# Kernel tuning notes

Hardware: AMD Instinct MI355X
Metric: run time of the kernel (lower is better)

The kernel has to match this reference:

```python
import jax, jax.numpy as jnp
import numpy as np

K = 3
PAD = 1


def conv2d(x, w, b, pad):
    y = jax.lax.conv_general_dilated(
        x, w, window_strides=(1, 1), padding=[(pad, pad), (pad, pad)],
        dimension_numbers=("NCHW", "OIHW", "NCHW"))
    return y + b[None, :, None, None]


def dcn_v2(f, w_off, b_off, w, b):
    # Modulated deformable conv (DCNv2), stride=1, pad=1, dilation=1, dg=1.
    B, C, H, W = f.shape
    om = conv2d(f, w_off, b_off, PAD)                 # [B, 27, H, W]
    o1, o2, m = jnp.split(om, 3, axis=1)
    offset = jnp.concatenate([o1, o2], axis=1).reshape(B, K * K, 2, H, W)
    dy, dx = offset[:, :, 0], offset[:, :, 1]          # [B, 9, H, W]
    mask = jax.nn.sigmoid(m)                           # [B, 9, H, W]
    ky = (jnp.arange(K * K) // K).astype(f.dtype)      # kernel row per tap
    kx = (jnp.arange(K * K) % K).astype(f.dtype)       # kernel col per tap
    hh = jnp.arange(H, dtype=f.dtype)
    ww = jnp.arange(W, dtype=f.dtype)
    ys = hh[None, None, :, None] - PAD + ky[None, :, None, None] + dy  # [B,9,H,W]
    xs = ww[None, None, None, :] - PAD + kx[None, :, None, None] + dx
    y0 = jnp.floor(ys)
    x0 = jnp.floor(xs)
    wy1 = ys - y0
    wx1 = xs - x0
    wy0 = 1.0 - wy1
    wx0 = 1.0 - wx1
    f_flat = f.reshape(B, C, H * W)

    def gather(yi, xi):
        valid = (yi >= 0) & (yi <= H - 1) & (xi >= 0) & (xi <= W - 1)
        yc = jnp.clip(yi, 0, H - 1).astype(jnp.int32)
        xc = jnp.clip(xi, 0, W - 1).astype(jnp.int32)
        idx = (yc * W + xc).reshape(B, 1, -1)          # [B,1,9*H*W]
        g = jnp.take_along_axis(f_flat, idx, axis=2).reshape(B, C, K * K, H, W)
        return g * valid.astype(f.dtype).reshape(B, 1, K * K, H, W)

    v = (gather(y0, x0) * (wy0 * wx0)[:, None]
         + gather(y0, x0 + 1) * (wy0 * wx1)[:, None]
         + gather(y0 + 1, x0) * (wy1 * wx0)[:, None]
         + gather(y0 + 1, x0 + 1) * (wy1 * wx1)[:, None])   # [B,C,9,H,W]
    v = v * mask[:, None]
    out = jnp.einsum("bckhw,ock->bohw", v, w.reshape(w.shape[0], C, K * K))
    return out + b[None, :, None, None]


def setup_inputs() -> dict:
    key = jax.random.key(0)
    ks = jax.random.split(key, 10)
    B, C, H, W = 2, 256, 128, 128
    s = 0.05
    return {
        "x": jax.random.normal(ks[0], (B, C, H, W), jnp.float32),
        "votes": jax.random.normal(ks[1], (B, C, H, W), jnp.float32),
        "w1": jax.random.normal(ks[2], (C, C, 3, 3), jnp.float32) * s,
        "b1": jnp.zeros((C,), jnp.float32),
        "w_off": jax.random.normal(ks[3], (27, C, 3, 3), jnp.float32) * 0.01,
        "b_off": jnp.zeros((27,), jnp.float32),
        "w_dcn": jax.random.normal(ks[4], (C, C, 3, 3), jnp.float32) * s,
        "b_dcn": jnp.zeros((C,), jnp.float32),
        "w2": jax.random.normal(ks[5], (C, C, 3, 3), jnp.float32) * s,
        "b2": jnp.zeros((C,), jnp.float32),
        "w3": jax.random.normal(ks[6], (C, C, 3, 3), jnp.float32) * s,
        "b3": jnp.zeros((C,), jnp.float32),
        "w4": jax.random.normal(ks[7], (2, C, 1, 1), jnp.float32) * s,
        "b4": jnp.zeros((2,), jnp.float32),
    }


def reference(x, votes, w1, b1, w_off, b_off, w_dcn, b_dcn, w2, b2, w3, b3, w4, b4):
    v = jax.nn.relu(votes)
    t = jax.nn.relu(conv2d(v, w1, b1, PAD))            # conv3x3 + relu
    t = jax.nn.relu(dcn_v2(t, w_off, b_off, w_dcn, b_dcn))  # DCN + relu
    t = conv2d(t, w2, b2, PAD)                         # conv3x3 (no relu)
    g = t * x                                          # gated by x
    h = jax.nn.relu(conv2d(g, w3, b3, PAD))            # conv3x3 + relu
    out = conv2d(h, w4, b4, 0)                         # 1x1 -> outplanes
    return out
```

## Files before the change

### kernel.cpp

```cpp
#include <hip/hip_runtime.h>
#include <math.h>

typedef short short8 __attribute__((ext_vector_type(8)));
typedef float f32x4 __attribute__((ext_vector_type(4)));
typedef unsigned int uint4v __attribute__((ext_vector_type(4)));
typedef unsigned short ushort_t;

__device__ inline ushort_t f2bf(float f) {
    unsigned u = __builtin_bit_cast(unsigned, f);
    u = (u + 0x7fffu + ((u >> 16) & 1u)) >> 16;
    return (ushort_t)u;
}
__device__ inline float bf2f(ushort_t u) {
    return __builtin_bit_cast(float, (unsigned)u << 16);
}
__device__ inline void gload_lds16(const ushort_t* g, short* l) {
    __builtin_amdgcn_global_load_lds((const __attribute__((address_space(1))) unsigned int*)g,
                                     (__attribute__((address_space(3))) unsigned int*)l, 16, 0, 0);
}

__device__ inline void wpack_body(const float* __restrict__ w, ushort_t* __restrict__ wpk,
                                  int COUT, int NF, int bidLocal, int tid) {
    int T = bidLocal * 256 + tid;
    int lane = T & 63;
    int rest = T >> 6;
    int n = rest % NF;
    int kstep = rest / NF;
    int t = kstep >> 3, cc = kstep & 7;
    int oc = n * 16 + (lane & 15);
    int kk = (lane >> 4) * 8;
    short8 sv;
#pragma unroll
    for (int j = 0; j < 8; ++j) {
        int ci = cc * 32 + kk + j;
        float val = (oc < COUT) ? w[((size_t)oc * 256 + ci) * 9 + t] : 0.f;
        sv[j] = (short)f2bf(val);
    }
    *(short8*)&wpk[(size_t)T * 8] = sv;
}

__global__ __launch_bounds__(256)
void prep_all_kernel(const float* w1, ushort_t* wpk1,
                     const float* w_off, ushort_t* wpkO,
                     const float* w_dcn, ushort_t* wpkD,
                     const float* w2, ushort_t* wpk2,
                     const float* w3, ushort_t* wpk3,
                     ushort_t* zp,
                     const float* __restrict__ votes, const float* __restrict__ x,
                     ushort_t* __restrict__ aN, ushort_t* __restrict__ xN) {
    __shared__ short s[64 * 66];
    int bid = blockIdx.x, tid = threadIdx.x;
    if (bid < 288)       { wpack_body(w1,    wpk1, 256, 16, bid,        tid); return; }
    else if (bid < 324)  { wpack_body(w_off, wpkO, 27,  2,  bid - 288,  tid); return; }
    else if (bid < 612)  { wpack_body(w_dcn, wpkD, 256, 16, bid - 324,  tid); return; }
    else if (bid < 900)  { wpack_body(w2,    wpk2, 256, 16, bid - 612,  tid); return; }
    else if (bid < 1188) { wpack_body(w3,    wpk3, 256, 16, bid - 900,  tid); return; }
    else if (bid == 1188) { zp[tid] = 0; return; }
    int nb = bid - 1189;
    const int px0 = (nb & 255) * 64;
    const int ci0 = ((nb >> 8) & 3) * 64;
    const int z   = nb >> 10;
    const int b   = z & 1;
    const bool doRelu = (z < 2);
    const float* inb = (doRelu ? votes : x) + (size_t)b * 256 * 16384;
    ushort_t* ob = (doRelu ? aN : xN) + (size_t)b * 16384 * 256;
#pragma unroll
    for (int rep = 0; rep < 16; ++rep) {
        int cl = rep * 4 + (tid >> 6);
        int pl = tid & 63;
        float v = inb[(size_t)(ci0 + cl) * 16384 + px0 + pl];
        if (doRelu) v = fmaxf(v, 0.f);
        s[pl * 66 + cl] = (short)f2bf(v);
    }
    __syncthreads();
#pragma unroll
    for (int rep = 0; rep < 2; ++rep) {
        int c = rep * 256 + tid;
        int pl = c >> 3;
        int cl = (c & 7) * 8;
        *(short8*)&ob[(size_t)(px0 + pl) * 256 + ci0 + cl] = *(const short8*)&s[pl * 66 + cl];
    }
}

template<int TW, int OUTC, int EPI>
__global__ __launch_bounds__(512, 2)
void conv_mfma_kernel(const ushort_t* __restrict__ in, const ushort_t* __restrict__ wpk,
                      const float* __restrict__ bias, int coutReal,
                      const ushort_t* __restrict__ xin, ushort_t* __restrict__ outp,
                      const ushort_t* __restrict__ zp,
                      const float* __restrict__ w4g, const float* __restrict__ b4g,
                      float* __restrict__ out4)
{
    constexpr int NF = OUTC / 16;
    constexpr int NN = (NF < 4) ? NF : 4;
    constexpr int HWD = TW + 2;
    constexpr int HPX = 6 * HWD;
    constexpr int ROUNDS = (HPX * 4 + 511) / 512;
    constexpr int MW  = TW / 16;
    constexpr int MPW = TW / 8;
    constexpr int PITCH = OUTC + 4;
    union SM { short a[2][ROUNDS * 512 * 8]; float e[TW * PITCH]; };
    __shared__ __align__(16) SM sm;

    const int tid  = threadIdx.x;
    const int lane = tid & 63;
    const int wv   = tid >> 6;
    const int hi   = lane >> 4;
    const int lo   = lane & 15;
    const int pxg  = wv & 1;
    const int wn   = wv >> 1;
    const int wnu  = __builtin_amdgcn_readfirstlane(wn);
    const int x0 = blockIdx.x * TW;
    const int y0 = blockIdx.y * 4;
    const int b  = blockIdx.z;
    const ushort_t* inb = in + (size_t)b * 16384 * 256;

    const ushort_t* sptr[ROUNDS];
    int sstep[ROUNDS];
#pragma unroll
    for (int r = 0; r < ROUNDS; ++r) {
        int g = r * 512 + tid;
        int px = g >> 2, slot = g & 3;
        int hy = px / HWD, hx = px - hy * HWD;
        int gy = y0 - 1 + hy, gx = x0 - 1 + hx;
        bool ok = (px < HPX) && ((unsigned)gy < 128u) && ((unsigned)gx < 128u);
        int kk = (px ^ (px >> 2)) & 3;
        sptr[r] = ok ? (inb + (size_t)((gy << 7) + gx) * 256 + ((slot ^ kk) << 3))
                     : (zp + (slot << 3));
        sstep[r] = ok ? 32 : 0;
    }

    int pxh_base[MPW];
#pragma unroll
    for (int m = 0; m < MPW; ++m)
        pxh_base[m] = (2 * pxg + m / MW) * HWD + (m % MW) * 16 + lo;

    f32x4 acc[MPW][NN];
#pragma unroll
    for (int m = 0; m < MPW; ++m)
#pragma unroll
        for (int n = 0; n < NN; ++n) acc[m][n] = (f32x4){0.f, 0.f, 0.f, 0.f};

#pragma unroll
    for (int r = 0; r < ROUNDS; ++r)
        gload_lds16(sptr[r], &sm.a[0][(r * 512 + wv * 64) * 8]);
    __syncthreads();

    for (int cc = 0; cc < 8; ++cc) {
        const int buf = cc & 1;
        if (cc < 7) {
#pragma unroll
            for (int r = 0; r < ROUNDS; ++r)
                gload_lds16(sptr[r] + (size_t)(cc + 1) * sstep[r],
                            &sm.a[buf ^ 1][(r * 512 + wv * 64) * 8]);
        }
        if (NF >= 4 || wnu == 0) {
#pragma unroll
            for (int t = 0; t < 9; ++t) {
                const int ky = t / 3, kx = t % 3;
                short8 bf[NN];
#pragma unroll
                for (int n = 0; n < NN; ++n)
                    bf[n] = *(const short8*)&wpk[((size_t)((t * 8 + cc) * NF + wnu * NN + n) * 64 + lane) * 8];
                short8 af[MPW];
#pragma unroll
                for (int m = 0; m < MPW; ++m) {
                    int ph = pxh_base[m] + ky * HWD + kx;
                    int off = ph * 32 + ((hi ^ ((ph ^ (ph >> 2)) & 3)) << 3);
                    af[m] = *(const short8*)&sm.a[buf][off];
                }
#pragma unroll
                for (int m = 0; m < MPW; ++m)
#pragma unroll
                    for (int n = 0; n < NN; ++n)
                        acc[m][n] = __builtin_amdgcn_mfma_f32_16x16x32_bf16(af[m], bf[n], acc[m][n], 0, 0, 0);
            }
        }
        __syncthreads();
    }

    float br[NN];
#pragma unroll
    for (int n = 0; n < NN; ++n) {
        int oc = wn * (16 * NN) + n * 16 + lo;
        br[n] = (oc < coutReal) ? bias[oc] : 0.f;
    }
    const size_t obase = ((size_t)b * 16384 + (size_t)y0 * 128 + x0) * OUTC;
#pragma unroll
    for (int p = 0; p < 4; ++p) {
        if (pxg == (p >> 1) && (NF >= 4 || wnu == 0)) {
#pragma unroll
            for (int mm = 0; mm < MW; ++mm) {
                int m = (p & 1) * MW + mm;
#pragma unroll
                for (int n = 0; n < NN; ++n)
#pragma unroll
                    for (int r = 0; r < 4; ++r) {
                        int col = mm * 16 + hi * 4 + r;
                        float v = acc[m][n][r] + br[n];
                        if (EPI == 1 || EPI == 3) v = fmaxf(v, 0.f);
                        sm.e[col * PITCH + wn * (16 * NN) + n * 16 + lo] = v;
                    }
            }
        }
        __syncthreads();
        if constexpr (EPI == 3) {
            int col = tid >> 5;
            int ch  = tid & 31;
            f32x4 v0 = *(const f32x4*)&sm.e[col * PITCH + ch * 8];
            f32x4 v1 = *(const f32x4*)&sm.e[col * PITCH + ch * 8 + 4];
            float4 wa0 = *(const float4*)&w4g[ch * 8];
            float4 wa1 = *(const float4*)&w4g[ch * 8 + 4];
            float4 wb0 = *(const float4*)&w4g[256 + ch * 8];
            float4 wb1 = *(const float4*)&w4g[256 + ch * 8 + 4];
            float a0 = v0[0] * wa0.x + v0[1] * wa0.y + v0[2] * wa0.z + v0[3] * wa0.w
                     + v1[0] * wa1.x + v1[1] * wa1.y + v1[2] * wa1.z + v1[3] * wa1.w;
            float a1 = v0[0] * wb0.x + v0[1] * wb0.y + v0[2] * wb0.z + v0[3] * wb0.w
                     + v1[0] * wb1.x + v1[1] * wb1.y + v1[2] * wb1.z + v1[3] * wb1.w;
#pragma unroll
            for (int s = 16; s >= 1; s >>= 1) {
                a0 += __shfl_xor(a0, s);
                a1 += __shfl_xor(a1, s);
            }
            if (ch == 0) {
                size_t o = (size_t)b * 2 * 16384 + (size_t)(y0 + p) * 128 + x0 + col;
                out4[o]         = a0 + b4g[0];
                out4[o + 16384] = a1 + b4g[1];
            }
        } else {
            constexpr int CHUNKS = TW * OUTC / 8;
            for (int c = tid; c < CHUNKS; c += 512) {
                int col = c / (OUTC / 8);
                int ch = c % (OUTC / 8);
                f32x4 v0 = *(const f32x4*)&sm.e[col * PITCH + ch * 8];
                f32x4 v1 = *(const f32x4*)&sm.e[col * PITCH + ch * 8 + 4];
                size_t gidx = obase + ((size_t)p * 128 + col) * OUTC + ch * 8;
                if (EPI == 2) {
                    uint4v xu = *(const uint4v*)&xin[gidx];
#pragma unroll
                    for (int j = 0; j < 4; ++j) {
                        float xa = bf2f((ushort_t)(xu[j] & 0xffffu));
                        float xb = __builtin_bit_cast(float, xu[j] & 0xffff0000u);
                        if (j < 2) { v0[2 * j] *= xa; v0[2 * j + 1] *= xb; }
                        else       { v1[2 * (j - 2)] *= xa; v1[2 * (j - 2) + 1] *= xb; }
                    }
                }
                short8 s;
#pragma unroll
                for (int j = 0; j < 4; ++j) s[j] = (short)f2bf(v0[j]);
#pragma unroll
                for (int j = 0; j < 4; ++j) s[4 + j] = (short)f2bf(v1[j]);
                *(short8*)&outp[gidx] = s;
            }
        }
        __syncthreads();
    }
}

__device__ inline void corner8(uint4v u, float w, float* sv) {
#pragma unroll
    for (int j = 0; j < 4; ++j) {
        unsigned a = u[j];
        sv[2 * j]     = fmaf(w, __builtin_bit_cast(float, a << 16), sv[2 * j]);
        sv[2 * j + 1] = fmaf(w, __builtin_bit_cast(float, a & 0xffff0000u), sv[2 * j + 1]);
    }
}

__global__ __launch_bounds__(256, 2)
void dcn_mfma_kernel(const ushort_t* __restrict__ ft, const ushort_t* __restrict__ omt,
                     const ushort_t* __restrict__ wpk, const float* __restrict__ bias,
                     ushort_t* __restrict__ outp)
{
    union SM { short a[2][2][2048]; float e[16 * 264]; };
    __shared__ __align__(16) SM sm;

    const int tid  = threadIdx.x;
    const int lane = tid & 63;
    const int wv   = tid >> 6;
    const int hi   = lane >> 4;
    const int lo   = lane & 15;
    const int bid  = blockIdx.x;
    const int tile = (bid & 7) * 64 + (bid >> 3);
    const int b    = tile >> 8;
    const int rem  = tile & 255;
    const int y0   = (rem >> 3) * 4;
    const int x0   = (rem & 7) * 16;
    const ushort_t* fb = ft + (size_t)b * 16384 * 256;

    const int pxl = (wv << 4) | (lane >> 2);
    const int q   = lane & 3;

    float mw[9][4];
    unsigned mc[9];
    {
        const int py = y0 + (pxl >> 4), pxx = x0 + (pxl & 15);
        const ushort_t* omp = omt + ((size_t)b * 16384 + py * 128 + pxx) * 32;
        uint4v ow[4];
#pragma unroll
        for (int j = 0; j < 4; ++j) ow[j] = *(const uint4v*)(omp + j * 8);
        unsigned wbuf[14];
#pragma unroll
        for (int j = 0; j < 4; ++j)
#pragma unroll
            for (int e = 0; e < 4; ++e)
                if (j * 4 + e < 14) wbuf[j * 4 + e] = ow[j][e];
#pragma unroll
        for (int t = 0; t < 9; ++t) {
            float dy = bf2f((ushort_t)(wbuf[t] & 0xffffu));
            float dx = bf2f((ushort_t)(wbuf[t] >> 16));
            unsigned mw_ = wbuf[(18 + t) >> 1];
            float mr = ((18 + t) & 1) ? bf2f((ushort_t)(mw_ >> 16)) : bf2f((ushort_t)(mw_ & 0xffffu));
            float mk = 1.f / (1.f + expf(-mr));
            float ys = (float)(py - 1 + t / 3) + dy;
            float xs = (float)(pxx - 1 + t % 3) + dx;
            float y0f = floorf(ys), x0f = floorf(xs);
            float wy1 = ys - y0f, wx1 = xs - x0f;
            float wy0 = 1.f - wy1, wx0 = 1.f - wx1;
            int yi = (int)y0f, xi = (int)x0f;
            bool vy0 = (yi >= 0) && (yi < 128), vy1 = (yi + 1 >= 0) && (yi + 1 < 128);
            bool vx0 = (xi >= 0) && (xi < 128), vx1 = (xi + 1 >= 0) && (xi + 1 < 128);
            mw[t][0] = (vy0 && vx0) ? wy0 * wx0 * mk : 0.f;
            mw[t][1] = (vy0 && vx1) ? wy0 * wx1 * mk : 0.f;
            mw[t][2] = (vy1 && vx0) ? wy1 * wx0 * mk : 0.f;
            mw[t][3] = (vy1 && vx1) ? wy1 * wx1 * mk : 0.f;
            int y0c = min(max(yi, 0), 127), y1c = min(max(yi + 1, 0), 127);
            int x0c = min(max(xi, 0), 127), x1c = min(max(xi + 1, 0), 127);
            mc[t] = (unsigned)y0c | ((unsigned)y1c << 8) | ((unsigned)x0c << 16) | ((unsigned)x1c << 24);
        }
    }

    const int w_off = pxl * 32 + ((q ^ ((pxl ^ (pxl >> 2)) & 3)) << 3);
    int a_off[4];
#pragma unroll
    for (int m = 0; m < 4; ++m) {
        int p_ = m * 16 + lo;
        a_off[m] = p_ * 32 + ((hi ^ ((p_ ^ (p_ >> 2)) & 3)) << 3);
    }

    f32x4 acc[4][4];
#pragma unroll
    for (int m = 0; m < 4; ++m)
#pragma unroll
        for (int n = 0; n < 4; ++n) acc[m][n] = (f32x4){0.f, 0.f, 0.f, 0.f};

    uint4v n0a, n0b, n0c, n0d;
    uint4v n1a, n1b, n1c, n1d;

    {
        unsigned c = mc[0];
        int yy0 = c & 255, yy1 = (c >> 8) & 255, xx0 = (c >> 16) & 255, xx1 = c >> 24;
        size_t o00 = (size_t)((yy0 << 7) + xx0) * 256, o01 = (size_t)((yy0 << 7) + xx1) * 256;
        size_t o10 = (size_t)((yy1 << 7) + xx0) * 256, o11 = (size_t)((yy1 << 7) + xx1) * 256;
#pragma unroll
        for (int h = 0; h < 2; ++h) {
            const ushort_t* pc = fb + h * 32 + q * 8;
            uint4v g0 = *(const uint4v*)(pc + o00);
            uint4v g1 = *(const uint4v*)(pc + o01);
            uint4v g2 = *(const uint4v*)(pc + o10);
            uint4v g3 = *(const uint4v*)(pc + o11);
            float sv[8] = {0.f, 0.f, 0.f, 0.f, 0.f, 0.f, 0.f, 0.f};
            corner8(g0, mw[0][0], sv); corner8(g1, mw[0][1], sv);
            corner8(g2, mw[0][2], sv); corner8(g3, mw[0][3], sv);
            unsigned pk[4];
#pragma unroll
            for (int j = 0; j < 4; ++j)
                asm("v_cvt_pk_bf16_f32 %0, %1, %2" : "=v"(pk[j]) : "v"(sv[2 * j]), "v"(sv[2 * j + 1]));
            *(uint4v*)&sm.a[0][h][w_off] = (uint4v){pk[0], pk[1], pk[2], pk[3]};
        }
    }
    __syncthreads();

    for (int cch = 0; cch < 4; ++cch) {
#pragma unroll
        for (int t = 0; t < 9; ++t) {
            const int cur = (cch + t) & 1;
            const bool last = (cch == 3) && (t == 8);
            const int tn   = (t == 8) ? 0 : t + 1;
            const int cchn = (t == 8) ? cch + 1 : cch;
            if (!last) {
                unsigned c = mc[tn];
                int yy0 = c & 255, yy1 = (c >> 8) & 255, xx0 = (c >> 16) & 255, xx1 = c >> 24;
                size_t o00 = (size_t)((yy0 << 7) + xx0) * 256, o01 = (size_t)((yy0 << 7) + xx1) * 256;
                size_t o10 = (size_t)((yy1 << 7) + xx0) * 256, o11 = (size_t)((yy1 << 7) + xx1) * 256;
                const ushort_t* pc0 = fb + (2 * cchn) * 32 + q * 8;
                n0a = *(const uint4v*)(pc0 + o00);
                n0b = *(const uint4v*)(pc0 + o01);
                n0c = *(const uint4v*)(pc0 + o10);
                n0d = *(const uint4v*)(pc0 + o11);
                const ushort_t* pc1 = pc0 + 32;
                n1a = *(const uint4v*)(pc1 + o00);
                n1b = *(const uint4v*)(pc1 + o01);
                n1c = *(const uint4v*)(pc1 + o10);
                n1d = *(const uint4v*)(pc1 + o11);
            }
            short8 bfr0[4], bfr1[4];
            {
                const ushort_t* bs0 = wpk + ((size_t)((t * 8 + 2 * cch) * 16 + wv * 4) * 64 + lane) * 8;
#pragma unroll
                for (int n = 0; n < 4; ++n)
                    bfr0[n] = *(const short8*)(bs0 + (size_t)n * 512);
                const ushort_t* bs1 = bs0 + 16 * 512;
#pragma unroll
                for (int n = 0; n < 4; ++n)
                    bfr1[n] = *(const short8*)(bs1 + (size_t)n * 512);
            }
#pragma unroll
            for (int m = 0; m < 4; ++m) {
                short8 af0 = *(const short8*)&sm.a[cur][0][a_off[m]];
                short8 af1 = *(const short8*)&sm.a[cur][1][a_off[m]];
#pragma unroll
                for (int n = 0; n < 4; ++n)
                    acc[m][n] = __builtin_amdgcn_mfma_f32_16x16x32_bf16(af0, bfr0[n], acc[m][n], 0, 0, 0);
#pragma unroll
                for (int n = 0; n < 4; ++n)
                    acc[m][n] = __builtin_amdgcn_mfma_f32_16x16x32_bf16(af1, bfr1[n], acc[m][n], 0, 0, 0);
            }
            if (!last) {
                {
                    float sv[8] = {0.f, 0.f, 0.f, 0.f, 0.f, 0.f, 0.f, 0.f};
                    corner8(n0a, mw[tn][0], sv); corner8(n0b, mw[tn][1], sv);
                    corner8(n0c, mw[tn][2], sv); corner8(n0d, mw[tn][3], sv);
                    unsigned pk[4];
#pragma unroll
                    for (int j = 0; j < 4; ++j)
                        asm("v_cvt_pk_bf16_f32 %0, %1, %2" : "=v"(pk[j]) : "v"(sv[2 * j]), "v"(sv[2 * j + 1]));
                    *(uint4v*)&sm.a[cur ^ 1][0][w_off] = (uint4v){pk[0], pk[1], pk[2], pk[3]};
                }
                {
                    float sv[8] = {0.f, 0.f, 0.f, 0.f, 0.f, 0.f, 0.f, 0.f};
                    corner8(n1a, mw[tn][0], sv); corner8(n1b, mw[tn][1], sv);
                    corner8(n1c, mw[tn][2], sv); corner8(n1d, mw[tn][3], sv);
                    unsigned pk[4];
#pragma unroll
                    for (int j = 0; j < 4; ++j)
                        asm("v_cvt_pk_bf16_f32 %0, %1, %2" : "=v"(pk[j]) : "v"(sv[2 * j]), "v"(sv[2 * j + 1]));
                    *(uint4v*)&sm.a[cur ^ 1][1][w_off] = (uint4v){pk[0], pk[1], pk[2], pk[3]};
                }
            }
            __syncthreads();
        }
    }

    float br[4];
#pragma unroll
    for (int n = 0; n < 4; ++n) br[n] = bias[wv * 64 + n * 16 + lo];
#pragma unroll
    for (int p = 0; p < 4; ++p) {
#pragma unroll
        for (int n = 0; n < 4; ++n)
#pragma unroll
            for (int r = 0; r < 4; ++r)
                sm.e[(hi * 4 + r) * 264 + wv * 64 + n * 16 + lo] = fmaxf(acc[p][n][r] + br[n], 0.f);
        __syncthreads();
#pragma unroll
        for (int j = 0; j < 2; ++j) {
            int c2 = j * 256 + tid;
            int pl = c2 >> 5, ch = c2 & 31;
            f32x4 v0 = *(const f32x4*)&sm.e[pl * 264 + ch * 8];
            f32x4 v1 = *(const f32x4*)&sm.e[pl * 264 + ch * 8 + 4];
            short8 s;
#pragma unroll
            for (int jj = 0; jj < 4; ++jj) s[jj] = (short)f2bf(v0[jj]);
#pragma unroll
            for (int jj = 0; jj < 4; ++jj) s[4 + jj] = (short)f2bf(v1[jj]);
            *(short8*)&outp[((size_t)b * 16384 + (size_t)(y0 + p) * 128 + x0 + pl) * 256 + ch * 8] = s;
        }
        __syncthreads();
    }
}

extern "C" void kernel_launch(void* const* d_in, const int* in_sizes, int n_in,
                              void* d_out, int out_size, void* d_ws, size_t ws_size,
                              hipStream_t stream) {
    const float* x     = (const float*)d_in[0];
    const float* votes = (const float*)d_in[1];
    const float* w1    = (const float*)d_in[2];
    const float* b1    = (const float*)d_in[3];
    const float* w_off = (const float*)d_in[4];
    const float* b_off = (const float*)d_in[5];
    const float* w_dcn = (const float*)d_in[6];
    const float* b_dcn = (const float*)d_in[7];
    const float* w2    = (const float*)d_in[8];
    const float* b2    = (const float*)d_in[9];
    const float* w3    = (const float*)d_in[10];
    const float* b3    = (const float*)d_in[11];
    const float* w4    = (const float*)d_in[12];
    const float* b4    = (const float*)d_in[13];
    float* outp = (float*)d_out;

    const int B = 2;
    const size_t featN = (size_t)B * 16384 * 256;

    ushort_t* ws   = (ushort_t*)d_ws;
    ushort_t* t1   = ws;
    ushort_t* t2   = t1 + featN;
    ushort_t* aN   = t2 + featN;
    ushort_t* xN   = aN + featN;
    ushort_t* om   = xN + featN;
    ushort_t* wpk1 = om + (size_t)B * 16384 * 32;
    ushort_t* wpkO = wpk1 + 589824;
    ushort_t* wpkD = wpkO + 73728;
    ushort_t* wpk2 = wpkD + 589824;
    ushort_t* wpk3 = wpk2 + 589824;
    ushort_t* zp   = wpk3 + 589824;

    prep_all_kernel<<<1189 + 4096, 256, 0, stream>>>(w1, wpk1, w_off, wpkO, w_dcn, wpkD,
                                                     w2, wpk2, w3, wpk3, zp, votes, x, aN, xN);

    dim3 cg16(8, 32, B);
    conv_mfma_kernel<16, 256, 1><<<cg16, 512, 0, stream>>>(aN, wpk1, b1, 256, nullptr, t1, zp, nullptr, nullptr, nullptr);
    conv_mfma_kernel<16, 32, 0><<<cg16, 512, 0, stream>>>(t1, wpkO, b_off, 27, nullptr, om, zp, nullptr, nullptr, nullptr);
    dcn_mfma_kernel<<<512, 256, 0, stream>>>(t1, om, wpkD, b_dcn, t2);
    conv_mfma_kernel<16, 256, 2><<<cg16, 512, 0, stream>>>(t2, wpk2, b2, 256, xN, aN, zp, nullptr, nullptr, nullptr);
    conv_mfma_kernel<16, 256, 3><<<cg16, 512, 0, stream>>>(aN, wpk3, b3, 256, nullptr, nullptr, zp, w4, b4, outp);
}
```

Baseline: 241.3 us.

## Split DCN kernel work across 512 threads with 8 waves per tile

The DCN kernel now runs 512 threads per block instead of 256. Each thread gathers one half of the 64-channel chunk instead of both halves, and each wave computes 32 output channels instead of 64. This halves per-thread gather loads, bilinear math and accumulators, which should lower register pressure and raise the number of waves available to hide gather latency. In exchange, each wave reloads the shared A tiles for fewer MFMAs, and more waves contend at each barrier.

Result: slower. 275.3 us (+14.1%).

```diff
diff --git a/kernel.cpp b/kernel.cpp
--- a/kernel.cpp
+++ b/kernel.cpp
@@ -266,7 +266,7 @@
     }
 }
 
-__global__ __launch_bounds__(256, 2)
+__global__ __launch_bounds__(512, 4)
 void dcn_mfma_kernel(const ushort_t* __restrict__ ft, const ushort_t* __restrict__ omt,
                      const ushort_t* __restrict__ wpk, const float* __restrict__ bias,
                      ushort_t* __restrict__ outp)
@@ -287,8 +287,9 @@
     const int x0   = (rem & 7) * 16;
     const ushort_t* fb = ft + (size_t)b * 16384 * 256;
 
-    const int pxl = (wv << 4) | (lane >> 2);
-    const int q   = lane & 3;
+    const int q   = tid & 3;
+    const int hc  = (tid >> 2) & 1;
+    const int pxl = tid >> 3;
 
     float mw[9][4];
     unsigned mc[9];
@@ -337,36 +338,30 @@
         a_off[m] = p_ * 32 + ((hi ^ ((p_ ^ (p_ >> 2)) & 3)) << 3);
     }
 
-    f32x4 acc[4][4];
+    f32x4 acc[4][2];
 #pragma unroll
     for (int m = 0; m < 4; ++m)
 #pragma unroll
-        for (int n = 0; n < 4; ++n) acc[m][n] = (f32x4){0.f, 0.f, 0.f, 0.f};
-
-    uint4v n0a, n0b, n0c, n0d;
-    uint4v n1a, n1b, n1c, n1d;
+        for (int n = 0; n < 2; ++n) acc[m][n] = (f32x4){0.f, 0.f, 0.f, 0.f};
+
+    uint4v na, nb, nc, nd;
 
     {
         unsigned c = mc[0];
         int yy0 = c & 255, yy1 = (c >> 8) & 255, xx0 = (c >> 16) & 255, xx1 = c >> 24;
-        size_t o00 = (size_t)((yy0 << 7) + xx0) * 256, o01 = (size_t)((yy0 << 7) + xx1) * 256;
-        size_t o10 = (size_t)((yy1 << 7) + xx0) * 256, o11 = (size_t)((yy1 << 7) + xx1) * 256;
-#pragma unroll
-        for (int h = 0; h < 2; ++h) {
-            const ushort_t* pc = fb + h * 32 + q * 8;
-            uint4v g0 = *(const uint4v*)(pc + o00);
-            uint4v g1 = *(const uint4v*)(pc + o01);
-            uint4v g2 = *(const uint4v*)(pc + o10);
-            uint4v g3 = *(const uint4v*)(pc + o11);
-            float sv[8] = {0.f, 0.f, 0.f, 0.f, 0.f, 0.f, 0.f, 0.f};
-            corner8(g0, mw[0][0], sv); corner8(g1, mw[0][1], sv);
-            corner8(g2, mw[0][2], sv); corner8(g3, mw[0][3], sv);
-            unsigned pk[4];
-#pragma unroll
-            for (int j = 0; j < 4; ++j)
-                asm("v_cvt_pk_bf16_f32 %0, %1, %2" : "=v"(pk[j]) : "v"(sv[2 * j]), "v"(sv[2 * j + 1]));
-            *(uint4v*)&sm.a[0][h][w_off] = (uint4v){pk[0], pk[1], pk[2], pk[3]};
-        }
+        const ushort_t* pc = fb + hc * 32 + q * 8;
+        na = *(const uint4v*)(pc + (size_t)((yy0 << 7) + xx0) * 256);
+        nb = *(const uint4v*)(pc + (size_t)((yy0 << 7) + xx1) * 256);
+        nc = *(const uint4v*)(pc + (size_t)((yy1 << 7) + xx0) * 256);
+        nd = *(const uint4v*)(pc + (size_t)((yy1 << 7) + xx1) * 256);
+        float sv[8] = {0.f, 0.f, 0.f, 0.f, 0.f, 0.f, 0.f, 0.f};
+        corner8(na, mw[0][0], sv); corner8(nb, mw[0][1], sv);
+        corner8(nc, mw[0][2], sv); corner8(nd, mw[0][3], sv);
+        unsigned pk[4];
+#pragma unroll
+        for (int j = 0; j < 4; ++j)
+            asm("v_cvt_pk_bf16_f32 %0, %1, %2" : "=v"(pk[j]) : "v"(sv[2 * j]), "v"(sv[2 * j + 1]));
+        *(uint4v*)&sm.a[0][hc][w_off] = (uint4v){pk[0], pk[1], pk[2], pk[3]};
     }
     __syncthreads();
 
@@ -380,28 +375,21 @@
             if (!last) {
                 unsigned c = mc[tn];
                 int yy0 = c & 255, yy1 = (c >> 8) & 255, xx0 = (c >> 16) & 255, xx1 = c >> 24;
-                size_t o00 = (size_t)((yy0 << 7) + xx0) * 256, o01 = (size_t)((yy0 << 7) + xx1) * 256;
-                size_t o10 = (size_t)((yy1 << 7) + xx0) * 256, o11 = (size_t)((yy1 << 7) + xx1) * 256;
-                const ushort_t* pc0 = fb + (2 * cchn) * 32 + q * 8;
-                n0a = *(const uint4v*)(pc0 + o00);
-                n0b = *(const uint4v*)(pc0 + o01);
-                n0c = *(const uint4v*)(pc0 + o10);
-                n0d = *(const uint4v*)(pc0 + o11);
-                const ushort_t* pc1 = pc0 + 32;
-                n1a = *(const uint4v*)(pc1 + o00);
-                n1b = *(const uint4v*)(pc1 + o01);
-                n1c = *(const uint4v*)(pc1 + o10);
-                n1d = *(const uint4v*)(pc1 + o11);
-            }
-            short8 bfr0[4], bfr1[4];
+                const ushort_t* pc = fb + (2 * cchn + hc) * 32 + q * 8;
+                na = *(const uint4v*)(pc + (size_t)((yy0 << 7) + xx0) * 256);
+                nb = *(const uint4v*)(pc + (size_t)((yy0 << 7) + xx1) * 256);
+                nc = *(const uint4v*)(pc + (size_t)((yy1 << 7) + xx0) * 256);
+                nd = *(const uint4v*)(pc + (size_t)((yy1 << 7) + xx1) * 256);
+            }
+            short8 bfr0[2], bfr1[2];
             {
-                const ushort_t* bs0 = wpk + ((size_t)((t * 8 + 2 * cch) * 16 + wv * 4) * 64 + lane) * 8;
-#pragma unroll
-                for (int n = 0; n < 4; ++n)
+                const ushort_t* bs0 = wpk + ((size_t)((t * 8 + 2 * cch) * 16 + wv * 2) * 64 + lane) * 8;
+#pragma unroll
+                for (int n = 0; n < 2; ++n)
                     bfr0[n] = *(const short8*)(bs0 + (size_t)n * 512);
                 const ushort_t* bs1 = bs0 + 16 * 512;
 #pragma unroll
-                for (int n = 0; n < 4; ++n)
+                for (int n = 0; n < 2; ++n)
                     bfr1[n] = *(const short8*)(bs1 + (size_t)n * 512);
             }
 #pragma unroll
@@ -409,53 +397,39 @@
                 short8 af0 = *(const short8*)&sm.a[cur][0][a_off[m]];
                 short8 af1 = *(const short8*)&sm.a[cur][1][a_off[m]];
 #pragma unroll
-                for (int n = 0; n < 4; ++n)
+                for (int n = 0; n < 2; ++n)
                     acc[m][n] = __builtin_amdgcn_mfma_f32_16x16x32_bf16(af0, bfr0[n], acc[m][n], 0, 0, 0);
 #pragma unroll
-                for (int n = 0; n < 4; ++n)
+                for (int n = 0; n < 2; ++n)
                     acc[m][n] = __builtin_amdgcn_mfma_f32_16x16x32_bf16(af1, bfr1[n], acc[m][n], 0, 0, 0);
             }
             if (!last) {
-                {
-                    float sv[8] = {0.f, 0.f, 0.f, 0.f, 0.f, 0.f, 0.f, 0.f};
-                    corner8(n0a, mw[tn][0], sv); corner8(n0b, mw[tn][1], sv);
-                    corner8(n0c, mw[tn][2], sv); corner8(n0d, mw[tn][3], sv);
-                    unsigned pk[4];
-#pragma unroll
-                    for (int j = 0; j < 4; ++j)
-                        asm("v_cvt_pk_bf16_f32 %0, %1, %2" : "=v"(pk[j]) : "v"(sv[2 * j]), "v"(sv[2 * j + 1]));
-                    *(uint4v*)&sm.a[cur ^ 1][0][w_off] = (uint4v){pk[0], pk[1], pk[2], pk[3]};
-                }
-                {
-                    float sv[8] = {0.f, 0.f, 0.f, 0.f, 0.f, 0.f, 0.f, 0.f};
-                    corner8(n1a, mw[tn][0], sv); corner8(n1b, mw[tn][1], sv);
-                    corner8(n1c, mw[tn][2], sv); corner8(n1d, mw[tn][3], sv);
-                    unsigned pk[4];
-#pragma unroll
-                    for (int j = 0; j < 4; ++j)
-                        asm("v_cvt_pk_bf16_f32 %0, %1, %2" : "=v"(pk[j]) : "v"(sv[2 * j]), "v"(sv[2 * j + 1]));
-                    *(uint4v*)&sm.a[cur ^ 1][1][w_off] = (uint4v){pk[0], pk[1], pk[2], pk[3]};
-                }
+                float sv[8] = {0.f, 0.f, 0.f, 0.f, 0.f, 0.f, 0.f, 0.f};
+                corner8(na, mw[tn][0], sv); corner8(nb, mw[tn][1], sv);
+                corner8(nc, mw[tn][2], sv); corner8(nd, mw[tn][3], sv);
+                unsigned pk[4];
+#pragma unroll
+                for (int j = 0; j < 4; ++j)
+                    asm("v_cvt_pk_bf16_f32 %0, %1, %2" : "=v"(pk[j]) : "v"(sv[2 * j]), "v"(sv[2 * j + 1]));
+                *(uint4v*)&sm.a[cur ^ 1][hc][w_off] = (uint4v){pk[0], pk[1], pk[2], pk[3]};
             }
             __syncthreads();
         }
     }
 
-    float br[4];
-#pragma unroll
-    for (int n = 0; n < 4; ++n) br[n] = bias[wv * 64 + n * 16 + lo];
+    float br[2];
+#pragma unroll
+    for (int n = 0; n < 2; ++n) br[n] = bias[wv * 32 + n * 16 + lo];
 #pragma unroll
     for (int p = 0; p < 4; ++p) {
 #pragma unroll
-        for (int n = 0; n < 4; ++n)
+        for (int n = 0; n < 2; ++n)
 #pragma unroll
             for (int r = 0; r < 4; ++r)
-                sm.e[(hi * 4 + r) * 264 + wv * 64 + n * 16 + lo] = fmaxf(acc[p][n][r] + br[n], 0.f);
+                sm.e[(hi * 4 + r) * 264 + wv * 32 + n * 16 + lo] = fmaxf(acc[p][n][r] + br[n], 0.f);
         __syncthreads();
-#pragma unroll
-        for (int j = 0; j < 2; ++j) {
-            int c2 = j * 256 + tid;
-            int pl = c2 >> 5, ch = c2 & 31;
+        {
+            int pl = tid >> 5, ch = tid & 31;
             f32x4 v0 = *(const f32x4*)&sm.e[pl * 264 + ch * 8];
             f32x4 v1 = *(const f32x4*)&sm.e[pl * 264 + ch * 8 + 4];
             short8 s;
@@ -510,7 +484,7 @@
     dim3 cg16(8, 32, B);
     conv_mfma_kernel<16, 256, 1><<<cg16, 512, 0, stream>>>(aN, wpk1, b1, 256, nullptr, t1, zp, nullptr, nullptr, nullptr);
     conv_mfma_kernel<16, 32, 0><<<cg16, 512, 0, stream>>>(t1, wpkO, b_off, 27, nullptr, om, zp, nullptr, nullptr, nullptr);
-    dcn_mfma_kernel<<<512, 256, 0, stream>>>(t1, om, wpkD, b_dcn, t2);
+    dcn_mfma_kernel<<<512, 512, 0, stream>>>(t1, om, wpkD, b_dcn, t2);
     conv_mfma_kernel<16, 256, 2><<<cg16, 512, 0, stream>>>(t2, wpk2, b2, 256, xN, aN, zp, nullptr, nullptr, nullptr);
     conv_mfma_kernel<16, 256, 3><<<cg16, 512, 0, stream>>>(aN, wpk3, b3, 256, nullptr, nullptr, zp, w4, b4, outp);
 }
```
